# Optimization experiments

Hardware: AMD Instinct MI355X
Metric: run time of the kernel (lower is better)

Reference implementation:

```python
import jax, jax.numpy as jnp
import numpy as np

KSIZE = 3
PAD = KSIZE // 2


def _conv2d(x, w):
    # x: (N, C, H, W), w: (O, C, kh, kw), stride 1, same padding
    return jax.lax.conv_general_dilated(
        x, w, window_strides=(1, 1), padding=[(PAD, PAD), (PAD, PAD)],
        dimension_numbers=("NCHW", "OIHW", "NCHW"))


def setup_inputs() -> dict:
    key = jax.random.key(0)
    k1, k2, k3 = jax.random.split(key, 3)
    B, Sx, Sy, Cin, Co, H, Wd = 4, 1, 32, 32, 32, 128, 128
    target = jax.random.normal(k1, (B, Sx, Cin, H, Wd), dtype=jnp.float32)
    support = jax.random.normal(k2, (B, Sy, Cin, H, Wd), dtype=jnp.float32)
    # kaiming_normal fan_in = 2*Cin*k*k, leaky_relu gain ~ sqrt(2/(1+0.01^2))
    fan_in = 2 * Cin * KSIZE * KSIZE
    std = float(np.sqrt(2.0 / (1.0 + 0.01 ** 2)) / np.sqrt(fan_in))
    W = jax.random.normal(k3, (Co, 2 * Cin, KSIZE, KSIZE), dtype=jnp.float32) * std
    bias = jnp.zeros((Co,), dtype=jnp.float32)
    return {"target": target, "support": support, "W": W, "bias": bias}


def reference(target, support, W, bias):
    # CrossConv2d: conv over concat([x_repeated, y_repeated]) is linear in
    # channels, so split W into Wx|Wy, convolve each set once, broadcast-sum.
    B, Sx, Cx, H, Wd = target.shape
    Sy, Cy = support.shape[1], support.shape[2]
    Co = W.shape[0]
    Wx, Wy = W[:, :Cx], W[:, Cx:]
    cx = _conv2d(target.reshape(B * Sx, Cx, H, Wd), Wx).reshape(B, Sx, 1, Co, H, Wd)
    cy = _conv2d(support.reshape(B * Sy, Cy, H, Wd), Wy).reshape(B, 1, Sy, Co, H, Wd)
    xy = cx + cy + bias[None, None, None, :, None, None]  # (B, Sx, Sy, Co, H, W)
    interaction = xy[:, 0]                                # squeeze Sx==1 -> (B, Sy, Co, H, W)
    new_target = jnp.mean(interaction, axis=1, keepdims=True)
    return (new_target, interaction)
```

## Files before the change

kernel.cpp:

```cpp
#include <hip/hip_runtime.h>

typedef short bf16x8 __attribute__((ext_vector_type(8)));
typedef float f32x4  __attribute__((ext_vector_type(4)));

namespace {

constexpr int CIN = 32, CO = 32, Himg = 128, Wimg = 128, SY = 32, Bb = 4;
constexpr int IMG = Himg * Wimg;
constexpr int NT  = Bb * CO * IMG;
constexpr size_t IS = (size_t)IMG * CIN;
constexpr size_t WS_NEED = (size_t)(Bb * SY + Bb) * IS * 2;

__device__ __forceinline__ unsigned cvtpk(float lo, float hi) {
  unsigned r;
  asm("v_cvt_pk_bf16_f32 %0, %1, %2" : "=v"(r) : "v"(lo), "v"(hi));
  return r;
}

#define GLD16(g, l)                                                        \
  __builtin_amdgcn_global_load_lds(                                       \
      (const __attribute__((address_space(1))) void*)(g),                 \
      (__attribute__((address_space(3))) void*)(l), 16, 0, 0)

#define FENCE() asm volatile("" ::: "memory")
#define BARX()                          \
  do {                                  \
    FENCE();                            \
    __builtin_amdgcn_s_barrier();       \
    FENCE();                            \
    __builtin_amdgcn_sched_barrier(0);  \
  } while (0)
#define WAITV(n) asm volatile("s_waitcnt vmcnt(" #n ")" ::: "memory")

__device__ __forceinline__ void load_w(bf16x8 wf[9],
                                       const float* __restrict__ Wfull,
                                       int cioff, int m, int lane)
{
  const int lx = lane & 15, kc = lane >> 4;
  #pragma unroll
  for (int tap = 0; tap < 9; ++tap) {
    const float* base = Wfull + (size_t)((m * 16 + lx) * 64 + cioff + kc * 8) * 9 + tap;
    bf16x8 w;
    #pragma unroll
    for (int j = 0; j < 8; ++j) {
      unsigned u = __builtin_bit_cast(unsigned, base[j * 9]);
      w[j] = (short)((u + 0x7FFFu + ((u >> 16) & 1u)) >> 16);
    }
    wf[tap] = w;
  }
}

__global__ __launch_bounds__(256)
void transform_nhwc(const float* __restrict__ target,
                    const float* __restrict__ support,
                    unsigned short* __restrict__ ws)
{
  __shared__ unsigned lbuf[256 * 17];

  const int tid   = threadIdx.x;
  const int img   = blockIdx.x >> 6;
  const int chunk = blockIdx.x & 63;
  const float* src = (img < Bb * SY)
      ? support + (size_t)img * CIN * IMG
      : target  + (size_t)(img - Bb * SY) * CIN * IMG;
  const int y0 = chunk * 2;

  f32x4 a[4], bv[4];
  #pragma unroll
  for (int k = 0; k < 4; ++k) {
    const int task = tid + k * 256;
    const int c2 = task >> 6, quad = task & 63;
    const float* p = src + (size_t)(2 * c2) * IMG + y0 * Wimg + quad * 4;
    a[k]  = *reinterpret_cast<const f32x4*>(p);
    bv[k] = *reinterpret_cast<const f32x4*>(p + IMG);
  }
  #pragma unroll
  for (int k = 0; k < 4; ++k) {
    const int task = tid + k * 256;
    const int c2 = task >> 6, quad = task & 63;
    #pragma unroll
    for (int e = 0; e < 4; ++e) {
      const int px = quad * 4 + e;
      lbuf[px * 17 + (c2 ^ ((px >> 2) & 15))] = cvtpk(a[k][e], bv[k][e]);
    }
  }
  __syncthreads();

  #pragma unroll
  for (int k = 0; k < 4; ++k) {
    const int G = tid + k * 256;
    const int r  = G >> 9;
    const int kc = (G >> 7) & 3;
    const int px = G & 127;
    const int pl = r * 128 + px;
    uint4 v;
    unsigned* vp = reinterpret_cast<unsigned*>(&v);
    #pragma unroll
    for (int w = 0; w < 3 + 1; ++w)
      vp[w] = lbuf[pl * 17 + ((kc * 4 + w) ^ ((pl >> 2) & 15))];
    unsigned short* dst = ws + (size_t)img * IS + (size_t)(y0 + r) * 4096 + kc * 1024 + px * 8;
    *reinterpret_cast<uint4*>(dst) = v;
  }
}


__device__ __forceinline__ void stage_img(char* __restrict__ ldsbuf,
                                          const char* __restrict__ imgbase,
                                          int y, int w, int lane)
{
  #pragma unroll
  for (int j = 0; j < 4; ++j) {
    const int c = w * 4 + j;
    const int ri = c >> 3, kc4 = (c >> 1) & 3, half = c & 1;
    int sr = y - 1 + ri;
    sr = sr < 0 ? 0 : (sr > 127 ? 127 : sr);
    const char* src = imgbase + (size_t)sr * 8192 + kc4 * 2048 + half * 1024 + lane * 16;
    char* dst = ldsbuf + ri * 8192 + kc4 * 2048 + half * 1024;
    GLD16(src, dst);
  }
}

__device__ __forceinline__ bf16x8 ld_frag(const char* __restrict__ buf,
                                          int ri, int kc, int s)
{
  return *reinterpret_cast<const bf16x8*>(buf + ri * 8192 + kc * 2048 + s * 16);
}

__device__ __forceinline__ void conv_one(f32x4 acc[2][2],
                                         const char* __restrict__ buf,
                                         const bf16x8 wf[9],
                                         int sbase, int kc,
                                         bool rok0, bool rok3)
{
  #pragma unroll
  for (int ri = 0; ri < 4; ++ri) {
    bf16x8 F[6];
    {
      const int s = sbase - 1;
      const int sc = s < 0 ? 0 : s;
      bf16x8 v = ld_frag(buf, ri, kc, sc);
      if (s < 0) v = bf16x8{0, 0, 0, 0, 0, 0, 0, 0};
      F[0] = v;
    }
    F[1] = ld_frag(buf, ri, kc, sbase);
    F[2] = ld_frag(buf, ri, kc, sbase + 1);
    F[3] = ld_frag(buf, ri, kc, sbase + 15);
    F[4] = ld_frag(buf, ri, kc, sbase + 16);
    {
      const int s = sbase + 17;
      const int sc = s > 127 ? 127 : s;
      bf16x8 v = ld_frag(buf, ri, kc, sc);
      if (s > 127) v = bf16x8{0, 0, 0, 0, 0, 0, 0, 0};
      F[5] = v;
    }
    const bool u0 = (ri <= 2) && (ri != 0 || rok0);
    const bool u1 = (ri >= 1) && (ri != 3 || rok3);
    if (u0) {
      #pragma unroll
      for (int kx = 0; kx < 3; ++kx)
        #pragma unroll
        for (int n = 0; n < 2; ++n)
          acc[0][n] = __builtin_amdgcn_mfma_f32_16x16x32_bf16(wf[ri * 3 + kx], F[n * 3 + kx], acc[0][n], 0, 0, 0);
    }
    if (u1) {
      #pragma unroll
      for (int kx = 0; kx < 3; ++kx)
        #pragma unroll
        for (int n = 0; n < 2; ++n)
          acc[1][n] = __builtin_amdgcn_mfma_f32_16x16x32_bf16(wf[(ri - 1) * 3 + kx], F[n * 3 + kx], acc[1][n], 0, 0, 0);
    }
  }
}

__global__ __launch_bounds__(512, 4)
void conv_lds(const unsigned short* __restrict__ ws,
              const float* __restrict__ Wfull,
              const float* __restrict__ bias,
              float* __restrict__ out)
{
  __shared__ char lds[2 * 32768];

  const int tid = threadIdx.x, lane = tid & 63, w = tid >> 6;
  const int pxq = w & 3, m = w >> 2;
  const int lx = lane & 15, kc = lane >> 4;

  const int orig = blockIdx.x;
  const int eff  = (orig & 7) * 128 + (orig >> 3);
  const int yp  = eff & 63;
  const int syq = (eff >> 6) & 3;
  const int b   = eff >> 8;

  const int y  = yp * 2;
  const bool rok0 = (y > 0), rok3 = (y < 126);
  const int sbase = pxq * 32 + lx;

  const char* tgt  = (const char*)(ws + (size_t)(Bb * SY + b) * IS);
  const char* sup0 = (const char*)(ws + (size_t)(b * SY + syq * 8) * IS);

  bf16x8 wf[9];
  load_w(wf, Wfull, 0, m, lane);

  stage_img(lds, tgt, y, w, lane);
  WAITV(0);
  __syncthreads();

  f32x4 cx[2][2];
  #pragma unroll
  for (int r2 = 0; r2 < 2; ++r2)
    #pragma unroll
    for (int n = 0; n < 2; ++n) cx[r2][n] = f32x4{0.f, 0.f, 0.f, 0.f};
  conv_one(cx, lds, wf, sbase, kc, rok0, rok3);
  #pragma unroll
  for (int j = 0; j < 4; ++j) {
    const float bvv = bias[m * 16 + kc * 4 + j];
    #pragma unroll
    for (int r2 = 0; r2 < 2; ++r2)
      #pragma unroll
      for (int n = 0; n < 2; ++n) cx[r2][n][j] += bvv;
  }
  load_w(wf, Wfull, 32, m, lane);

  BARX();

  stage_img(lds,         sup0,                 y, w, lane);
  stage_img(lds + 32768, sup0 + (size_t)IS * 2, y, w, lane);
  WAITV(4);
  BARX();

  f32x4 sum[2][2];
  #pragma unroll
  for (int r2 = 0; r2 < 2; ++r2)
    #pragma unroll
    for (int n = 0; n < 2; ++n) sum[r2][n] = f32x4{0.f, 0.f, 0.f, 0.f};

  for (int i = 0; i < 8; ++i) {
    const char* cb = lds + (i & 1) * 32768;

    f32x4 acc[2][2];
    #pragma unroll
    for (int r2 = 0; r2 < 2; ++r2)
      #pragma unroll
      for (int n = 0; n < 2; ++n) acc[r2][n] = cx[r2][n];
    conv_one(acc, cb, wf, sbase, kc, rok0, rok3);

    const int sy = syq * 8 + i;
    #pragma unroll
    for (int r2 = 0; r2 < 2; ++r2)
      #pragma unroll
      for (int n = 0; n < 2; ++n) {
        sum[r2][n] += acc[r2][n];
        const size_t basei = (size_t)NT +
            (((size_t)(b * SY + sy) * CO + m * 16 + kc * 4) * Himg + y + r2) * Wimg +
            pxq * 32 + n * 16 + lx;
        #pragma unroll
        for (int j = 0; j < 4; ++j)
          out[basei + (size_t)j * IMG] = acc[r2][n][j];
      }

    BARX();
    if (i + 2 < 8)
      stage_img(lds + (i & 1) * 32768, sup0 + (size_t)(i + 2) * IS * 2, y, w, lane);
    WAITV(4);
    BARX();
  }

  #pragma unroll
  for (int r2 = 0; r2 < 2; ++r2)
    #pragma unroll
    for (int n = 0; n < 2; ++n) {
      const size_t baseo =
          ((size_t)(b * CO + m * 16 + kc * 4) * Himg + y + r2) * Wimg + pxq * 32 + n * 16 + lx;
      #pragma unroll
      for (int j = 0; j < 4; ++j) {
        const float cyPart = (sum[r2][n][j] - 8.f * cx[r2][n][j]) * (1.f / 32.f);
        const float v = cyPart + (syq == 0 ? cx[r2][n][j] : 0.f);
        atomicAdd(&out[baseo + (size_t)j * IMG], v);
      }
    }
}

constexpr int TROWS = 6, TQ = 17, TCOLS = 70;
constexpr int NPIX  = TROWS * TCOLS;
constexpr int LDSB  = NPIX * 64;
constexpr int RTASK = TROWS * TQ;
constexpr int FB_NTHR = 512;
constexpr int FB_TPT  = 4;
constexpr int FB_SYC  = 8;

__device__ __forceinline__ int fb_swz(int pix, int cb) {
  return (pix * 64 + cb) ^ ((pix & 7) << 4);
}
__device__ __forceinline__ void fb_task_decode(int t, int& ch, int& row, int& q, bool& act) {
  ch = t & 15;
  const int r = t >> 4;
  row = r / TQ;
  q   = r - row * TQ;
  act = (r < RTASK);
}
__device__ __forceinline__ void fb_stage_load(f32x4 va[FB_TPT], f32x4 vb[FB_TPT],
                                              const float* __restrict__ src,
                                              int y0, int xq0, int tid)
{
  #pragma unroll
  for (int k = 0; k < FB_TPT; ++k) {
    int ch, row, q; bool act;
    fb_task_decode(tid + k * FB_NTHR, ch, row, q, act);
    const int y = y0 - 1 + row;
    act = act && ((unsigned)y < (unsigned)Himg);
    f32x4 v0 = {0.f, 0.f, 0.f, 0.f}, v1 = {0.f, 0.f, 0.f, 0.f};
    if (act) {
      const float* p = src + (size_t)(2 * ch) * IMG + y * Wimg + 4 * (xq0 + q);
      v0 = *reinterpret_cast<const f32x4*>(p);
      v1 = *reinterpret_cast<const f32x4*>(p + IMG);
    }
    va[k] = v0; vb[k] = v1;
  }
}
__device__ __forceinline__ void fb_stage_write(const f32x4 va[FB_TPT], const f32x4 vb[FB_TPT],
                                               char* __restrict__ lds,
                                               int y0, int xq0, int x0, int tid)
{
  #pragma unroll
  for (int k = 0; k < FB_TPT; ++k) {
    int ch, row, q; bool act;
    fb_task_decode(tid + k * FB_NTHR, ch, row, q, act);
    const int y = y0 - 1 + row;
    act = act && ((unsigned)y < (unsigned)Himg);
    if (act) {
      const int ix0 = 4 * (xq0 + q) - x0 + 1;
      #pragma unroll
      for (int e = 0; e < 4; ++e) {
        const int ix = ix0 + e;
        if (ix >= 0) {
          const int pix = row * TCOLS + ix;
          *reinterpret_cast<unsigned*>(lds + fb_swz(pix, ch * 4)) =
              cvtpk(va[k][e], vb[k][e]);
        }
      }
    }
  }
}
__device__ __forceinline__ void fb_conv1(f32x4 acc[4],
                                         const char* __restrict__ lds,
                                         const bf16x8 wf[9],
                                         int row, int lane)
{
  const int lx = lane & 15, kc = lane >> 4;
  #pragma unroll
  for (int ky = 0; ky < 3; ++ky) {
    #pragma unroll
    for (int kx = 0; kx < 3; ++kx) {
      const int tap = ky * 3 + kx;
      #pragma unroll
      for (int n = 0; n < 4; ++n) {
        const int p = (row + ky) * TCOLS + n * 16 + lx + kx;
        const bf16x8 bfrag = *reinterpret_cast<const bf16x8*>(lds + fb_swz(p, kc * 16));
        acc[n] = __builtin_amdgcn_mfma_f32_16x16x32_bf16(wf[tap], bfrag, acc[n], 0, 0, 0);
      }
    }
  }
}
__global__ __launch_bounds__(FB_NTHR, 4)
void fb_cross_mfma(const float* __restrict__ target,
                   const float* __restrict__ support,
                   const float* __restrict__ Wfull,
                   const float* __restrict__ bias,
                   float* __restrict__ out)
{
  __shared__ char lds[LDSB];
  const int tid  = threadIdx.x;
  const int lane = tid & 63;
  const int wv   = tid >> 6;
  const int row  = wv & 3;
  const int m    = wv >> 2;
  const int lx = lane & 15, kc = lane >> 4;
  const int bid = blockIdx.x;
  const int syq = bid & 3;
  const int xh  = (bid >> 2) & 1;
  const int yb  = (bid >> 3) & 31;
  const int b   = bid >> 8;
  const int y0 = yb * 4, x0 = xh * 64;
  const int y  = y0 + row;
  const int xq0 = xh ? 15 : 0;

  for (int e = tid; e < NPIX * 4; e += FB_NTHR)
    reinterpret_cast<f32x4*>(lds)[e] = f32x4{0.f, 0.f, 0.f, 0.f};

  bf16x8 wf[9];
  load_w(wf, Wfull, 0, m, lane);
  f32x4 va[FB_TPT], vb[FB_TPT];
  fb_stage_load(va, vb, target + (size_t)b * CIN * IMG, y0, xq0, tid);
  __syncthreads();
  fb_stage_write(va, vb, lds, y0, xq0, x0, tid);
  __syncthreads();

  f32x4 cx[4];
  #pragma unroll
  for (int n = 0; n < 4; ++n) cx[n] = f32x4{0.f, 0.f, 0.f, 0.f};
  fb_conv1(cx, lds, wf, row, lane);
  #pragma unroll
  for (int j = 0; j < 4; ++j) {
    const float bvv = bias[m * 16 + kc * 4 + j];
    #pragma unroll
    for (int n = 0; n < 4; ++n) cx[n][j] += bvv;
  }

  const float* supp0 = support + (size_t)(b * SY + syq * FB_SYC) * CIN * IMG;
  fb_stage_load(va, vb, supp0, y0, xq0, tid);
  load_w(wf, Wfull, 32, m, lane);
  __syncthreads();
  fb_stage_write(va, vb, lds, y0, xq0, x0, tid);

  f32x4 sum[4];
  #pragma unroll
  for (int n = 0; n < 4; ++n) sum[n] = f32x4{0.f, 0.f, 0.f, 0.f};
  __syncthreads();

  for (int i = 0; i < FB_SYC; ++i) {
    if (i < FB_SYC - 1)
      fb_stage_load(va, vb, supp0 + (size_t)(i + 1) * CIN * IMG, y0, xq0, tid);

    f32x4 acc[4];
    #pragma unroll
    for (int n = 0; n < 4; ++n) acc[n] = cx[n];
    fb_conv1(acc, lds, wf, row, lane);
    __syncthreads();

    if (i < FB_SYC - 1)
      fb_stage_write(va, vb, lds, y0, xq0, x0, tid);

    const int sy = syq * FB_SYC + i;
    #pragma unroll
    for (int n = 0; n < 4; ++n) {
      sum[n] += acc[n];
      const size_t basei = (size_t)NT +
          (((size_t)(b * SY + sy) * CO + m * 16 + kc * 4) * Himg + y) * Wimg +
          x0 + n * 16 + lx;
      #pragma unroll
      for (int j = 0; j < 4; ++j)
        out[basei + (size_t)j * IMG] = acc[n][j];
    }
    __syncthreads();
  }

  #pragma unroll
  for (int n = 0; n < 4; ++n) {
    const size_t baseo =
        ((size_t)(b * CO + m * 16 + kc * 4) * Himg + y) * Wimg + x0 + n * 16 + lx;
    #pragma unroll
    for (int j = 0; j < 4; ++j) {
      const float cyPart = (sum[n][j] - (float)FB_SYC * cx[n][j]) * (1.f / 32.f);
      const float v = cyPart + (syq == 0 ? cx[n][j] : 0.f);
      atomicAdd(&out[baseo + (size_t)j * IMG], v);
    }
  }
}

}

extern "C" void kernel_launch(void* const* d_in, const int* in_sizes, int n_in,
                              void* d_out, int out_size, void* d_ws, size_t ws_size,
                              hipStream_t stream)
{
  (void)in_sizes; (void)n_in; (void)out_size;
  const float* target  = (const float*)d_in[0];
  const float* support = (const float*)d_in[1];
  const float* Wfull   = (const float*)d_in[2];
  const float* bias    = (const float*)d_in[3];
  float* out = (float*)d_out;

  hipMemsetAsync(d_out, 0, (size_t)NT * sizeof(float), stream);

  if (ws_size >= WS_NEED) {
    unsigned short* ws = (unsigned short*)d_ws;
    transform_nhwc<<<dim3((Bb * SY + Bb) * 64), 256, 0, stream>>>(target, support, ws);
    conv_lds<<<dim3(1024), 512, 0, stream>>>(ws, Wfull, bias, out);
  } else {
    fb_cross_mfma<<<dim3(1024), FB_NTHR, 0, stream>>>(target, support, Wfull, bias, out);
  }
}
```

Before: 267.5 us.

## Compute new_target by convolving a precomputed support mean instead of atomics

Adds a kernel that averages the 32 bf16 support images per batch into an extra workspace image. One quarter of the conv blocks then convolve this mean image as a ninth image and write new_target directly. This removes the output memset and the atomicAdd reduction, at the cost of an extra launch, a full read of the support workspace, and extra conv work on some blocks, which creates load imbalance. Rounding the averaged support to bf16 also changes numerics slightly.

Measured after the change: 242.2 us (median of 2 runs). 1.1x faster.

```diff
diff --git a/kernel.cpp b/kernel.cpp
--- a/kernel.cpp
+++ b/kernel.cpp
@@ -9,7 +9,8 @@
 constexpr int IMG = Himg * Wimg;
 constexpr int NT  = Bb * CO * IMG;
 constexpr size_t IS = (size_t)IMG * CIN;
-constexpr size_t WS_NEED = (size_t)(Bb * SY + Bb) * IS * 2;
+constexpr size_t WS1 = (size_t)132 * IS * 2;
+constexpr size_t WS2 = (size_t)136 * IS * 2;
 
 __device__ __forceinline__ unsigned cvtpk(float lo, float hi) {
   unsigned r;
@@ -96,11 +97,50 @@
     uint4 v;
     unsigned* vp = reinterpret_cast<unsigned*>(&v);
     #pragma unroll
-    for (int w = 0; w < 3 + 1; ++w)
+    for (int w = 0; w < 4; ++w)
       vp[w] = lbuf[pl * 17 + ((kc * 4 + w) ^ ((pl >> 2) & 15))];
     unsigned short* dst = ws + (size_t)img * IS + (size_t)(y0 + r) * 4096 + kc * 1024 + px * 8;
     *reinterpret_cast<uint4*>(dst) = v;
   }
+}
+
+__global__ __launch_bounds__(256)
+void mean_k(unsigned short* __restrict__ ws)
+{
+  const int b = blockIdx.x >> 7, y = blockIdx.x & 127;
+  const size_t off = (size_t)y * 4096 + threadIdx.x * 16;
+
+  float s[16];
+  #pragma unroll
+  for (int k = 0; k < 16; ++k) s[k] = 0.f;
+
+  #pragma unroll 4
+  for (int sy = 0; sy < SY; ++sy) {
+    const uint4* p = reinterpret_cast<const uint4*>(ws + (size_t)(b * SY + sy) * IS + off);
+    uint4 v0 = p[0], v1 = p[1];
+    const unsigned* w0 = reinterpret_cast<const unsigned*>(&v0);
+    const unsigned* w1 = reinterpret_cast<const unsigned*>(&v1);
+    #pragma unroll
+    for (int q = 0; q < 4; ++q) {
+      s[2 * q + 0] += __builtin_bit_cast(float, w0[q] << 16);
+      s[2 * q + 1] += __builtin_bit_cast(float, w0[q] & 0xffff0000u);
+      s[8 + 2 * q + 0] += __builtin_bit_cast(float, w1[q] << 16);
+      s[8 + 2 * q + 1] += __builtin_bit_cast(float, w1[q] & 0xffff0000u);
+    }
+  }
+
+  constexpr float inv = 1.0f / SY;
+  uint4 o0, o1;
+  unsigned* q0 = reinterpret_cast<unsigned*>(&o0);
+  unsigned* q1 = reinterpret_cast<unsigned*>(&o1);
+  #pragma unroll
+  for (int q = 0; q < 4; ++q) {
+    q0[q] = cvtpk(s[2 * q] * inv, s[2 * q + 1] * inv);
+    q1[q] = cvtpk(s[8 + 2 * q] * inv, s[8 + 2 * q + 1] * inv);
+  }
+  uint4* dst = reinterpret_cast<uint4*>(ws + (size_t)(132 + b) * IS + off);
+  dst[0] = o0;
+  dst[1] = o1;
 }
 
 
@@ -172,6 +212,7 @@
   }
 }
 
+template <bool NTMEAN>
 __global__ __launch_bounds__(512, 4)
 void conv_lds(const unsigned short* __restrict__ ws,
               const float* __restrict__ Wfull,
@@ -196,6 +237,10 @@
 
   const char* tgt  = (const char*)(ws + (size_t)(Bb * SY + b) * IS);
   const char* sup0 = (const char*)(ws + (size_t)(b * SY + syq * 8) * IS);
+  const char* mnp  = (const char*)(ws + (size_t)(132 + b) * IS);
+
+  const bool doNT = NTMEAN && (syq == (yp & 3));
+  const int nimg = doNT ? 9 : 8;
 
   bf16x8 wf[9];
   load_w(wf, Wfull, 0, m, lane);
@@ -222,18 +267,20 @@
 
   BARX();
 
-  stage_img(lds,         sup0,                 y, w, lane);
+  stage_img(lds,         sup0,                  y, w, lane);
   stage_img(lds + 32768, sup0 + (size_t)IS * 2, y, w, lane);
   WAITV(4);
   BARX();
 
   f32x4 sum[2][2];
-  #pragma unroll
-  for (int r2 = 0; r2 < 2; ++r2)
-    #pragma unroll
-    for (int n = 0; n < 2; ++n) sum[r2][n] = f32x4{0.f, 0.f, 0.f, 0.f};
-
-  for (int i = 0; i < 8; ++i) {
+  if constexpr (!NTMEAN) {
+    #pragma unroll
+    for (int r2 = 0; r2 < 2; ++r2)
+      #pragma unroll
+      for (int n = 0; n < 2; ++n) sum[r2][n] = f32x4{0.f, 0.f, 0.f, 0.f};
+  }
+
+  for (int i = 0; i < nimg; ++i) {
     const char* cb = lds + (i & 1) * 32768;
 
     f32x4 acc[2][2];
@@ -243,40 +290,58 @@
       for (int n = 0; n < 2; ++n) acc[r2][n] = cx[r2][n];
     conv_one(acc, cb, wf, sbase, kc, rok0, rok3);
 
-    const int sy = syq * 8 + i;
-    #pragma unroll
-    for (int r2 = 0; r2 < 2; ++r2)
-      #pragma unroll
-      for (int n = 0; n < 2; ++n) {
-        sum[r2][n] += acc[r2][n];
-        const size_t basei = (size_t)NT +
-            (((size_t)(b * SY + sy) * CO + m * 16 + kc * 4) * Himg + y + r2) * Wimg +
-            pxq * 32 + n * 16 + lx;
+    if (!NTMEAN || i < 8) {
+      const int sy = syq * 8 + i;
+      #pragma unroll
+      for (int r2 = 0; r2 < 2; ++r2)
         #pragma unroll
-        for (int j = 0; j < 4; ++j)
-          out[basei + (size_t)j * IMG] = acc[r2][n][j];
-      }
+        for (int n = 0; n < 2; ++n) {
+          if constexpr (!NTMEAN) sum[r2][n] += acc[r2][n];
+          const size_t basei = (size_t)NT +
+              (((size_t)(b * SY + sy) * CO + m * 16 + kc * 4) * Himg + y + r2) * Wimg +
+              pxq * 32 + n * 16 + lx;
+          #pragma unroll
+          for (int j = 0; j < 4; ++j)
+            out[basei + (size_t)j * IMG] = acc[r2][n][j];
+        }
+    } else {
+      #pragma unroll
+      for (int r2 = 0; r2 < 2; ++r2)
+        #pragma unroll
+        for (int n = 0; n < 2; ++n) {
+          const size_t baseo =
+              ((size_t)(b * CO + m * 16 + kc * 4) * Himg + y + r2) * Wimg +
+              pxq * 32 + n * 16 + lx;
+          #pragma unroll
+          for (int j = 0; j < 4; ++j)
+            out[baseo + (size_t)j * IMG] = acc[r2][n][j];
+        }
+    }
 
     BARX();
-    if (i + 2 < 8)
-      stage_img(lds + (i & 1) * 32768, sup0 + (size_t)(i + 2) * IS * 2, y, w, lane);
+    if (i + 2 < nimg) {
+      const char* nsrc = (i + 2 < 8) ? sup0 + (size_t)(i + 2) * IS * 2 : mnp;
+      stage_img(lds + (i & 1) * 32768, nsrc, y, w, lane);
+    }
     WAITV(4);
     BARX();
   }
 
-  #pragma unroll
-  for (int r2 = 0; r2 < 2; ++r2)
-    #pragma unroll
-    for (int n = 0; n < 2; ++n) {
-      const size_t baseo =
-          ((size_t)(b * CO + m * 16 + kc * 4) * Himg + y + r2) * Wimg + pxq * 32 + n * 16 + lx;
-      #pragma unroll
-      for (int j = 0; j < 4; ++j) {
-        const float cyPart = (sum[r2][n][j] - 8.f * cx[r2][n][j]) * (1.f / 32.f);
-        const float v = cyPart + (syq == 0 ? cx[r2][n][j] : 0.f);
-        atomicAdd(&out[baseo + (size_t)j * IMG], v);
+  if constexpr (!NTMEAN) {
+    #pragma unroll
+    for (int r2 = 0; r2 < 2; ++r2)
+      #pragma unroll
+      for (int n = 0; n < 2; ++n) {
+        const size_t baseo =
+            ((size_t)(b * CO + m * 16 + kc * 4) * Himg + y + r2) * Wimg + pxq * 32 + n * 16 + lx;
+        #pragma unroll
+        for (int j = 0; j < 4; ++j) {
+          const float cyPart = (sum[r2][n][j] - 8.f * cx[r2][n][j]) * (1.f / 32.f);
+          const float v = cyPart + (syq == 0 ? cx[r2][n][j] : 0.f);
+          atomicAdd(&out[baseo + (size_t)j * IMG], v);
+        }
       }
-    }
+  }
 }
 
 constexpr int TROWS = 6, TQ = 17, TCOLS = 70;
@@ -469,13 +534,18 @@
   const float* bias    = (const float*)d_in[3];
   float* out = (float*)d_out;
 
-  hipMemsetAsync(d_out, 0, (size_t)NT * sizeof(float), stream);
-
-  if (ws_size >= WS_NEED) {
+  if (ws_size >= WS2) {
     unsigned short* ws = (unsigned short*)d_ws;
     transform_nhwc<<<dim3((Bb * SY + Bb) * 64), 256, 0, stream>>>(target, support, ws);
-    conv_lds<<<dim3(1024), 512, 0, stream>>>(ws, Wfull, bias, out);
+    mean_k<<<dim3(512), 256, 0, stream>>>(ws);
+    conv_lds<true><<<dim3(1024), 512, 0, stream>>>(ws, Wfull, bias, out);
+  } else if (ws_size >= WS1) {
+    unsigned short* ws = (unsigned short*)d_ws;
+    hipMemsetAsync(d_out, 0, (size_t)NT * sizeof(float), stream);
+    transform_nhwc<<<dim3((Bb * SY + Bb) * 64), 256, 0, stream>>>(target, support, ws);
+    conv_lds<false><<<dim3(1024), 512, 0, stream>>>(ws, Wfull, bias, out);
   } else {
+    hipMemsetAsync(d_out, 0, (size_t)NT * sizeof(float), stream);
     fb_cross_mfma<<<dim3(1024), FB_NTHR, 0, stream>>>(target, support, Wfull, bias, out);
   }
 }
```
